# Kernel optimization log

Measured on AMD Instinct MI355X. Metric: run time of the kernel, lower is better.

The kernel has to match this reference:

```python
import jax, jax.numpy as jnp
import numpy as np

IN_CHANNELS = 256
OUT_CHANNELS = 256
KERNEL_SIZE = 3
CHANNELS_PER_FILTER = 32
B, H, W = 4, 56, 56


def setup_inputs() -> dict:
    key = jax.random.key(0)
    k1, k2, k3 = jax.random.split(key, 3)
    x = jax.random.normal(k1, (B, IN_CHANNELS, H, W), dtype=jnp.float32)
    # kaiming-uniform-ish scale: bound = 1/sqrt(fan_in)
    fan_in = CHANNELS_PER_FILTER * KERNEL_SIZE ** 2
    bound = 1.0 / np.sqrt(fan_in)
    weight = jax.random.uniform(
        k2, (OUT_CHANNELS, CHANNELS_PER_FILTER, KERNEL_SIZE, KERNEL_SIZE),
        dtype=jnp.float32, minval=-bound, maxval=bound)
    connections = jax.random.randint(
        k3, (OUT_CHANNELS, CHANNELS_PER_FILTER), 0, IN_CHANNELS, dtype=jnp.int32)
    return {"x": x, "weight": weight, "connections": connections}


def reference(x, weight, connections):
    # x: (B, Cin, H, W); weight: (O, cpf, k, k); connections: (O, cpf) int32
    B_, O, cpf = x.shape[0], weight.shape[0], weight.shape[1]
    Hh, Ww = x.shape[2], x.shape[3]
    # Gather each filter's input-channel subset: (B, O, cpf, H, W)
    gathered = x[:, connections]
    # Grouped conv: each of the O groups convolves its cpf channels.
    gathered = gathered.reshape(B_, O * cpf, Hh, Ww)
    out = jax.lax.conv_general_dilated(
        gathered, weight,
        window_strides=(1, 1), padding="SAME",
        dimension_numbers=("NCHW", "OIHW", "NCHW"),
        feature_group_count=O)
    return out  # (B, O, H, W)
```

## Files before the change

### kernel.cpp

```cpp
#include <hip/hip_runtime.h>
#include <stdint.h>

#define NPIX 3136
#define OC 256
#define IC 256
#define CPF 32
#define BUF_FLOATS 3456
#define ZROW 3360

typedef const __attribute__((address_space(1))) uint32_t* gptr_t;
typedef __attribute__((address_space(3))) uint32_t* lptr_t;

__device__ __forceinline__ float dpp_shr1(float v) {
    return __int_as_float(__builtin_amdgcn_update_dpp(
        0, __float_as_int(v), 0x111, 0xF, 0xF, true));
}
__device__ __forceinline__ float dpp_shl1(float v) {
    return __int_as_float(__builtin_amdgcn_update_dpp(
        0, __float_as_int(v), 0x101, 0xF, 0xF, true));
}

__global__ __launch_bounds__(256, 4) void sparse_conv_kernel(
    const float* __restrict__ x, const float* __restrict__ weight,
    const int* __restrict__ connections, float* __restrict__ out)
{
    __shared__ __align__(16) float buf[2][BUF_FLOATS];

    const int bid = blockIdx.x;
    const int b = bid & 3;
    const int o = bid >> 2;
    const int t = threadIdx.x;
    const int lane = t & 63;
    const int wv = t >> 6;

    if (t < 64) { buf[0][ZROW + t] = 0.f; buf[1][ZROW + t] = 0.f; }

    const int cbase = (wv == 0) ? 0 : (3 * wv + 1);
    const int cnum  = (wv == 0) ? 4 : 3;

    const float* xb   = x + (size_t)b * IC * NPIX;
    const int*   conn = connections + o * CPF;
    const float* wo   = weight + o * CPF * 9;

    const int s = t & 15;
    const int g = t >> 4;
    const bool active = (g < 14);

    {
        const float* plane = xb + (size_t)conn[0] * NPIX;
        for (int i = 0; i < cnum; ++i) {
            const int chunk = cbase + i;
            int goff = chunk * 256 + lane * 4;
            if (goff > 3132) goff = 3132;
            __builtin_amdgcn_global_load_lds((gptr_t)(plane + goff),
                                             (lptr_t)(&buf[0][chunk * 256]),
                                             16, 0, 0);
        }
    }
    __syncthreads();

    float4 acc[4];
#pragma unroll
    for (int r = 0; r < 4; ++r) acc[r] = make_float4(0.f, 0.f, 0.f, 0.f);

    int cur = 0;
    for (int c = 0; c < CPF; ++c) {
        if (c + 1 < CPF) {
            const float* plane = xb + (size_t)conn[c + 1] * NPIX;
            float* dst = &buf[cur ^ 1][0];
            for (int i = 0; i < cnum; ++i) {
                const int chunk = cbase + i;
                int goff = chunk * 256 + lane * 4;
                if (goff > 3132) goff = 3132;
                __builtin_amdgcn_global_load_lds((gptr_t)(plane + goff),
                                                 (lptr_t)(dst + chunk * 256),
                                                 16, 0, 0);
            }
        }

        float wt[9];
#pragma unroll
        for (int k = 0; k < 9; ++k) wt[k] = wo[c * 9 + k];

        if (active) {
            const float* bp = &buf[cur][0];
#pragma unroll
            for (int k = 0; k < 6; ++k) {
                const int rr = 4 * g - 1 + k;
                const int rc = ((unsigned)rr < 56u) ? rr * 56 : ZROW;
                const float4 m = *reinterpret_cast<const float4*>(bp + rc + 4 * s);
                const float L = dpp_shr1(m.w);
                float       R = dpp_shl1(m.x);
                R = (s == 13) ? 0.f : R;
#pragma unroll
                for (int r = 0; r < 4; ++r) {
                    const int kh = k - r;
                    if (kh >= 0 && kh < 3) {
                        const float w0 = wt[kh * 3 + 0];
                        const float w1 = wt[kh * 3 + 1];
                        const float w2 = wt[kh * 3 + 2];
                        acc[r].x += w0 * L    + w1 * m.x + w2 * m.y;
                        acc[r].y += w0 * m.x  + w1 * m.y + w2 * m.z;
                        acc[r].z += w0 * m.y  + w1 * m.z + w2 * m.w;
                        acc[r].w += w0 * m.z  + w1 * m.w + w2 * R;
                    }
                }
            }
        }

        __syncthreads();
        cur ^= 1;
    }

    if (active && s < 14) {
        float* ob = out + ((size_t)b * OC + o) * NPIX + (4 * g) * 56 + 4 * s;
#pragma unroll
        for (int r = 0; r < 4; ++r)
            *reinterpret_cast<float4*>(ob + r * 56) = acc[r];
    }
}

extern "C" void kernel_launch(void* const* d_in, const int* in_sizes, int n_in,
                              void* d_out, int out_size, void* d_ws, size_t ws_size,
                              hipStream_t stream) {
    const float* x    = (const float*)d_in[0];
    const float* wgt  = (const float*)d_in[1];
    const int*   conn = (const int*)d_in[2];
    float* out = (float*)d_out;

    dim3 grid(4 * OC);
    dim3 block(256);
    hipLaunchKernelGGL(sparse_conv_kernel, grid, block, 0, stream, x, wgt, conn, out);
}
```

Measured before the change: 119.1 us.

## Load input rows directly into registers with double-buffered prefetch instead of LDS

Removes the shared-memory staging buffer and the async global-to-LDS copies. Each thread now loads its six needed rows per channel straight from global memory into registers. A two-deep register ping-pong prefetches the next channel while computing the current one. This drops the per-channel __syncthreads barrier and LDS traffic, but rows are re-read from global/L2 by overlapping thread groups (halo rows read three times) and register pressure rises.

```diff
diff --git a/kernel.cpp b/kernel.cpp
--- a/kernel.cpp
+++ b/kernel.cpp
@@ -5,11 +5,6 @@
 #define OC 256
 #define IC 256
 #define CPF 32
-#define BUF_FLOATS 3456
-#define ZROW 3360
-
-typedef const __attribute__((address_space(1))) uint32_t* gptr_t;
-typedef __attribute__((address_space(3))) uint32_t* lptr_t;
 
 __device__ __forceinline__ float dpp_shr1(float v) {
     return __int_as_float(__builtin_amdgcn_update_dpp(
@@ -24,74 +19,51 @@
     const float* __restrict__ x, const float* __restrict__ weight,
     const int* __restrict__ connections, float* __restrict__ out)
 {
-    __shared__ __align__(16) float buf[2][BUF_FLOATS];
-
     const int bid = blockIdx.x;
     const int b = bid & 3;
     const int o = bid >> 2;
     const int t = threadIdx.x;
-    const int lane = t & 63;
-    const int wv = t >> 6;
-
-    if (t < 64) { buf[0][ZROW + t] = 0.f; buf[1][ZROW + t] = 0.f; }
-
-    const int cbase = (wv == 0) ? 0 : (3 * wv + 1);
-    const int cnum  = (wv == 0) ? 4 : 3;
+    const int s = t & 15;
+    const int g = t >> 4;
+    const bool active = (g < 14);
 
     const float* xb   = x + (size_t)b * IC * NPIX;
     const int*   conn = connections + o * CPF;
     const float* wo   = weight + o * CPF * 9;
 
-    const int s = t & 15;
-    const int g = t >> 4;
-    const bool active = (g < 14);
-
-    {
-        const float* plane = xb + (size_t)conn[0] * NPIX;
-        for (int i = 0; i < cnum; ++i) {
-            const int chunk = cbase + i;
-            int goff = chunk * 256 + lane * 4;
-            if (goff > 3132) goff = 3132;
-            __builtin_amdgcn_global_load_lds((gptr_t)(plane + goff),
-                                             (lptr_t)(&buf[0][chunk * 256]),
-                                             16, 0, 0);
-        }
+    int off[6]; bool mk[6];
+#pragma unroll
+    for (int k = 0; k < 6; ++k) {
+        const int rr = 4 * g - 1 + k;
+        const int rc = rr < 0 ? 0 : (rr > 55 ? 55 : rr);
+        off[k] = rc * 56 + 4 * s;
+        mk[k] = ((unsigned)rr < 56u) && active;
     }
-    __syncthreads();
+    const bool redge = (s == 13);
 
     float4 acc[4];
 #pragma unroll
     for (int r = 0; r < 4; ++r) acc[r] = make_float4(0.f, 0.f, 0.f, 0.f);
 
-    int cur = 0;
-    for (int c = 0; c < CPF; ++c) {
-        if (c + 1 < CPF) {
-            const float* plane = xb + (size_t)conn[c + 1] * NPIX;
-            float* dst = &buf[cur ^ 1][0];
-            for (int i = 0; i < cnum; ++i) {
-                const int chunk = cbase + i;
-                int goff = chunk * 256 + lane * 4;
-                if (goff > 3132) goff = 3132;
-                __builtin_amdgcn_global_load_lds((gptr_t)(plane + goff),
-                                                 (lptr_t)(dst + chunk * 256),
-                                                 16, 0, 0);
-            }
-        }
+    auto loadrows = [&](int c, float4* m) {
+        const float* plane = xb + (size_t)conn[c] * NPIX;
+#pragma unroll
+        for (int k = 0; k < 6; ++k)
+            m[k] = *reinterpret_cast<const float4*>(plane + off[k]);
+    };
 
+    auto compute = [&](const float4* m, int c) {
+        const float* wp = wo + c * 9;
         float wt[9];
 #pragma unroll
-        for (int k = 0; k < 9; ++k) wt[k] = wo[c * 9 + k];
-
-        if (active) {
-            const float* bp = &buf[cur][0];
+        for (int i = 0; i < 9; ++i) wt[i] = wp[i];
 #pragma unroll
-            for (int k = 0; k < 6; ++k) {
-                const int rr = 4 * g - 1 + k;
-                const int rc = ((unsigned)rr < 56u) ? rr * 56 : ZROW;
-                const float4 m = *reinterpret_cast<const float4*>(bp + rc + 4 * s);
-                const float L = dpp_shr1(m.w);
-                float       R = dpp_shl1(m.x);
-                R = (s == 13) ? 0.f : R;
+        for (int k = 0; k < 6; ++k) {
+            if (mk[k]) {
+                const float4 mm = m[k];
+                const float L = dpp_shr1(mm.w);
+                float       R = dpp_shl1(mm.x);
+                R = redge ? 0.f : R;
 #pragma unroll
                 for (int r = 0; r < 4; ++r) {
                     const int kh = k - r;
@@ -99,17 +71,25 @@
                         const float w0 = wt[kh * 3 + 0];
                         const float w1 = wt[kh * 3 + 1];
                         const float w2 = wt[kh * 3 + 2];
-                        acc[r].x += w0 * L    + w1 * m.x + w2 * m.y;
-                        acc[r].y += w0 * m.x  + w1 * m.y + w2 * m.z;
-                        acc[r].z += w0 * m.y  + w1 * m.z + w2 * m.w;
-                        acc[r].w += w0 * m.z  + w1 * m.w + w2 * R;
+                        acc[r].x += w0 * L    + w1 * mm.x + w2 * mm.y;
+                        acc[r].y += w0 * mm.x + w1 * mm.y + w2 * mm.z;
+                        acc[r].z += w0 * mm.y + w1 * mm.z + w2 * mm.w;
+                        acc[r].w += w0 * mm.z + w1 * mm.w + w2 * R;
                     }
                 }
             }
         }
+    };
 
-        __syncthreads();
-        cur ^= 1;
+    float4 mA[6], mB[6];
+    loadrows(0, mA);
+#pragma unroll 1
+    for (int it = 0; it < 16; ++it) {
+        const int c = 2 * it;
+        loadrows(c + 1, mB);
+        compute(mA, c);
+        if (it < 15) loadrows(c + 2, mA);
+        compute(mB, c + 1);
     }
 
     if (active && s < 14) {
```

New measurement: 114.8 us. 1.04x faster.
